# Kernel optimization log

Measured on AMD Instinct MI355X. Metric: run time of the kernel, lower is better.

## Reference

```python
import jax, jax.numpy as jnp
import numpy as np

MIN_RANGE = -128.0
MAX_RANGE = 127.0


def quantize(t, min_range=MIN_RANGE, max_range=MAX_RANGE):
    """Per-tensor affine (asymmetric) quantization, as in QuantizedMatrix.
    Returns (q, scale, zero_point) with q in [min_range, max_range]."""
    mn = jnp.min(t)
    mx = jnp.max(t)
    scale = (mx - mn) / (max_range - min_range)
    zero_point = jnp.round(min_range - mn / scale)
    q = jnp.clip(jnp.round(t / scale) + zero_point, min_range, max_range)
    return q, scale, zero_point


def setup_inputs() -> dict:
    key = jax.random.key(0)
    k1, k2, k3 = jax.random.split(key, 3)
    B, S, D_IN, D_OUT = 4, 2048, 4096, 4096
    x = jax.random.normal(k1, (B, S, D_IN), dtype=jnp.float32)
    # nn.Linear weight layout: [out_features, in_features]
    W = jax.random.normal(k2, (D_OUT, D_IN), dtype=jnp.float32) * (1.0 / np.sqrt(D_IN))
    bias = jax.random.normal(k3, (D_OUT,), dtype=jnp.float32) * 0.02
    return {"x": x, "W": W, "bias": bias}


def reference(x, W, bias):
    # Quantize activations (per-tensor over the whole [B,S,D] tensor) and weights.
    qx, sx, zx = quantize(x)
    qw, sw, zw = quantize(W)
    # QuantizedMatrix matmul: dequantized product
    #   s_x * s_w * (q_x - z_x) @ (q_w - z_w)^T  , W is [out,in] so contract on 'd'.
    acc = jnp.einsum("bsd,od->bso", qx - zx, qw - zw)
    res = (sx * sw) * acc + bias
    return res
```

## Files before the change

kernel.cpp:

```cpp
#include <hip/hip_runtime.h>

#define GM 8192
#define GN 4096
#define GK 4096
#define NT (GK / 64)

#define QX_OFF   0ull
#define QW_OFF   33554432ull
#define RSX_OFF  50331648ull
#define RSW_OFF  50364416ull
#define PRM_OFF  50380832ull

#define MMB_X 2048
#define MMB_W 1024

using v4i  = __attribute__((ext_vector_type(4)))  int;
using v16i = __attribute__((ext_vector_type(16))) int;

__device__ __forceinline__ void async16(const signed char* g, signed char* l) {
    __builtin_amdgcn_global_load_lds((const __attribute__((address_space(1))) void*)g,
                                     (__attribute__((address_space(3))) void*)l,
                                     16, 0, 0);
}

__global__ void k_minmax(const float4* __restrict__ x, const float4* __restrict__ Wt,
                         float* __restrict__ part) {
    const float4* p; int n4, b0, nb; float* dst;
    if (blockIdx.x < MMB_X) { p = x;  n4 = GM * GK / 4; b0 = blockIdx.x;         nb = MMB_X; dst = part;        }
    else                    { p = Wt; n4 = GN * GK / 4; b0 = blockIdx.x - MMB_X; nb = MMB_W; dst = part + 4096; }
    float mx = -3.4e38f, mn = 3.4e38f;
    for (int i = b0 * 256 + threadIdx.x; i < n4; i += nb * 256) {
        float4 v = p[i];
        mx = fmaxf(mx, fmaxf(fmaxf(v.x, v.y), fmaxf(v.z, v.w)));
        mn = fminf(mn, fminf(fminf(v.x, v.y), fminf(v.z, v.w)));
    }
    #pragma unroll
    for (int o = 32; o > 0; o >>= 1) {
        mx = fmaxf(mx, __shfl_down(mx, o));
        mn = fminf(mn, __shfl_down(mn, o));
    }
    __shared__ float smx[4], smn[4];
    int w = threadIdx.x >> 6;
    if ((threadIdx.x & 63) == 0) { smx[w] = mx; smn[w] = mn; }
    __syncthreads();
    if (threadIdx.x == 0) {
        #pragma unroll
        for (int i = 1; i < 4; i++) { mx = fmaxf(mx, smx[i]); mn = fminf(mn, smn[i]); }
        dst[b0]      = mx;
        dst[nb + b0] = mn;
    }
}

__global__ void k_params(const float* __restrict__ part, float* prm) {
    const int t = threadIdx.x;
    float v0 = -3.4e38f, v1 = 3.4e38f, v2 = -3.4e38f, v3 = 3.4e38f;
    for (int i = t; i < MMB_X; i += 256) {
        v0 = fmaxf(v0, part[i]);
        v1 = fminf(v1, part[MMB_X + i]);
    }
    for (int i = t; i < MMB_W; i += 256) {
        v2 = fmaxf(v2, part[4096 + i]);
        v3 = fminf(v3, part[5120 + i]);
    }
    #pragma unroll
    for (int o = 32; o > 0; o >>= 1) {
        v0 = fmaxf(v0, __shfl_down(v0, o));
        v1 = fminf(v1, __shfl_down(v1, o));
        v2 = fmaxf(v2, __shfl_down(v2, o));
        v3 = fminf(v3, __shfl_down(v3, o));
    }
    __shared__ float s[4][4];
    const int wv = t >> 6;
    if ((t & 63) == 0) { s[wv][0] = v0; s[wv][1] = v1; s[wv][2] = v2; s[wv][3] = v3; }
    __syncthreads();
    if (t == 0) {
        #pragma unroll
        for (int i = 1; i < 4; i++) {
            v0 = fmaxf(v0, s[i][0]); v1 = fminf(v1, s[i][1]);
            v2 = fmaxf(v2, s[i][2]); v3 = fminf(v3, s[i][3]);
        }
        float sx  = (v0 - v1) / 255.0f;
        float zxf = rintf(-128.0f - v1 / sx);
        float sw  = (v2 - v3) / 255.0f;
        float zwf = rintf(-128.0f - v3 / sw);
        prm[0] = sx; prm[1] = zxf; prm[2] = sw; prm[3] = zwf; prm[4] = sx * sw;
        int* ip = (int*)prm;
        ip[5] = (int)zxf; ip[6] = (int)zwf;
    }
}

__global__ void k_quant(const float* __restrict__ x, const float* __restrict__ Wt,
                        signed char* __restrict__ qx, signed char* __restrict__ qw,
                        int* __restrict__ rsx, int* __restrict__ rsw,
                        const float* __restrict__ prm) {
    const float* src; signed char* q; int* rs; int pidx, row;
    if (blockIdx.x < GM) { row = blockIdx.x;      src = x;  q = qx; rs = rsx; pidx = 0; }
    else                 { row = blockIdx.x - GM; src = Wt; q = qw; rs = rsw; pidx = 2; }
    const int t = threadIdx.x;
    const float s  = prm[pidx];
    const float zp = prm[pidx + 1];
    const float4* srow = (const float4*)(src + (size_t)row * GK);
    int* qrow = (int*)(q + (size_t)row * GK);
    int acc = 0;
    #pragma unroll
    for (int i = 0; i < 4; i++) {
        float4 v = srow[i * 256 + t];
        int q0 = (int)fminf(fmaxf(rintf(v.x / s) + zp, -128.0f), 127.0f);
        int q1 = (int)fminf(fmaxf(rintf(v.y / s) + zp, -128.0f), 127.0f);
        int q2 = (int)fminf(fmaxf(rintf(v.z / s) + zp, -128.0f), 127.0f);
        int q3 = (int)fminf(fmaxf(rintf(v.w / s) + zp, -128.0f), 127.0f);
        acc += q0 + q1 + q2 + q3;
        qrow[i * 256 + t] = (q0 & 255) | ((q1 & 255) << 8) | ((q2 & 255) << 16)
                          | ((q3 & 255) << 24);
    }
    #pragma unroll
    for (int o = 32; o > 0; o >>= 1) acc += __shfl_down(acc, o);
    __shared__ int sa[4];
    if ((t & 63) == 0) sa[t >> 6] = acc;
    __syncthreads();
    if (t == 0) rs[row] = sa[0] + sa[1] + sa[2] + sa[3];
}

__global__ __launch_bounds__(512, 2) void k_gemm(
    const signed char* __restrict__ qx, const signed char* __restrict__ qw,
    const int* __restrict__ rsx, const int* __restrict__ rsw,
    const float* __restrict__ bias, const float* __restrict__ prm,
    float* __restrict__ out) {
    __shared__ __align__(16) signed char lds[3][2][256 * 64];

    const int tid  = threadIdx.x;
    const int lane = tid & 63;
    const int w    = tid >> 6;
    const int bid  = ((blockIdx.x & 7) << 6) | (blockIdx.x >> 3);
    const int tm0  = (bid >> 4) * 256;
    const int tn0  = (bid & 15) * 256;

    const int slab = w & 3;
    const int sr   = lane >> 2;
    const int sc   = ((lane & 3) ^ ((lane >> 3) & 3)) * 16;
    const signed char* gsrc = (w < 4)
        ? qx + (size_t)(tm0 + slab * 64 + sr) * GK + sc
        : qw + (size_t)(tn0 + slab * 64 + sr) * GK + sc;
    const int ldsTensor = (w < 4) ? 0 : 1;
    const int ldsSlab   = slab * 64 * 64;

    const int wr = w >> 2;
    const int wc = w & 3;
    const int fr = lane & 31;
    const int fh = lane >> 5;

    v16i acc[4][2] = {};
    v4i  fa[4], fb[2];

    auto LDF = [&](int bi, int s) {
        const signed char* cA = lds[bi][0];
        const signed char* cB = lds[bi][1];
        const int cc = s * 2 + fh;
        const int ca = (cc ^ ((fr >> 1) & 3)) * 16;
        fa[0] = *(const v4i*)(cA + (wr * 128      + fr) * 64 + ca);
        fa[1] = *(const v4i*)(cA + (wr * 128 + 32 + fr) * 64 + ca);
        fa[2] = *(const v4i*)(cA + (wr * 128 + 64 + fr) * 64 + ca);
        fa[3] = *(const v4i*)(cA + (wr * 128 + 96 + fr) * 64 + ca);
        fb[0] = *(const v4i*)(cB + (wc * 64       + fr) * 64 + ca);
        fb[1] = *(const v4i*)(cB + (wc * 64  + 32 + fr) * 64 + ca);
    };
    auto MM = [&]() {
        __builtin_amdgcn_s_setprio(1);
        acc[0][0] = __builtin_amdgcn_mfma_i32_32x32x32_i8(fa[0], fb[0], acc[0][0], 0, 0, 0);
        acc[0][1] = __builtin_amdgcn_mfma_i32_32x32x32_i8(fa[0], fb[1], acc[0][1], 0, 0, 0);
        acc[1][0] = __builtin_amdgcn_mfma_i32_32x32x32_i8(fa[1], fb[0], acc[1][0], 0, 0, 0);
        acc[1][1] = __builtin_amdgcn_mfma_i32_32x32x32_i8(fa[1], fb[1], acc[1][1], 0, 0, 0);
        acc[2][0] = __builtin_amdgcn_mfma_i32_32x32x32_i8(fa[2], fb[0], acc[2][0], 0, 0, 0);
        acc[2][1] = __builtin_amdgcn_mfma_i32_32x32x32_i8(fa[2], fb[1], acc[2][1], 0, 0, 0);
        acc[3][0] = __builtin_amdgcn_mfma_i32_32x32x32_i8(fa[3], fb[0], acc[3][0], 0, 0, 0);
        acc[3][1] = __builtin_amdgcn_mfma_i32_32x32x32_i8(fa[3], fb[1], acc[3][1], 0, 0, 0);
        __builtin_amdgcn_s_setprio(0);
    };

    #pragma unroll
    for (int j = 0; j < 4; j++)
        async16(gsrc + (size_t)j * 16 * GK, &lds[0][ldsTensor][ldsSlab + j * 1024]);
    #pragma unroll
    for (int j = 0; j < 4; j++)
        async16(gsrc + (size_t)j * 16 * GK + 64, &lds[1][ldsTensor][ldsSlab + j * 1024]);
    asm volatile("s_waitcnt vmcnt(4)" ::: "memory");
    __builtin_amdgcn_s_barrier();
    LDF(0, 0);

    int rd = 0;
    for (int kt = 0; kt < NT; ++kt) {
        int st = rd + 2; if (st >= 3) st -= 3;
        const int nrd = (rd + 1 == 3) ? 0 : rd + 1;
        const size_t ko = (size_t)(kt + 2) * 64;
        const bool stg = (kt < NT - 2);
        __builtin_amdgcn_s_barrier();
        asm volatile("s_waitcnt lgkmcnt(0)" ::: "memory");
        __builtin_amdgcn_sched_barrier(0);
        MM();
        LDF(rd, 1);
        if (stg) {
            async16(gsrc + (size_t)0 * 16 * GK + ko, &lds[st][ldsTensor][ldsSlab + 0 * 1024]);
            async16(gsrc + (size_t)1 * 16 * GK + ko, &lds[st][ldsTensor][ldsSlab + 1 * 1024]);
            asm volatile("s_waitcnt vmcnt(2)" ::: "memory");
        } else if (kt == NT - 2) {
            asm volatile("s_waitcnt vmcnt(0)" ::: "memory");
        }
        __builtin_amdgcn_s_barrier();
        asm volatile("s_waitcnt lgkmcnt(0)" ::: "memory");
        __builtin_amdgcn_sched_barrier(0);
        MM();
        if (kt < NT - 1) LDF(nrd, 0);
        if (stg) {
            async16(gsrc + (size_t)2 * 16 * GK + ko, &lds[st][ldsTensor][ldsSlab + 2 * 1024]);
            async16(gsrc + (size_t)3 * 16 * GK + ko, &lds[st][ldsTensor][ldsSlab + 3 * 1024]);
        }
        rd = nrd;
    }

    const float sxsw = prm[4];
    const int* ip = (const int*)prm;
    const int zxi = ip[5], zwi = ip[6];
    const int kzz = GK * zxi * zwi;
    #pragma unroll
    for (int i = 0; i < 4; i++) {
        #pragma unroll
        for (int j = 0; j < 2; j++) {
            const int col = tn0 + wc * 64 + j * 32 + fr;
            const int ccol = kzz - zxi * rsw[col];
            const float bv = bias[col];
            #pragma unroll
            for (int reg = 0; reg < 16; reg++) {
                const int row = tm0 + wr * 128 + i * 32
                              + (reg & 3) + 8 * (reg >> 2) + 4 * fh;
                const int t = acc[i][j][reg] - zwi * rsx[row] + ccol;
                out[(size_t)row * GN + col] = fmaf(sxsw, (float)t, bv);
            }
        }
    }
}

extern "C" void kernel_launch(void* const* d_in, const int* in_sizes, int n_in,
                              void* d_out, int out_size, void* d_ws, size_t ws_size,
                              hipStream_t stream) {
    const float* x    = (const float*)d_in[0];
    const float* Wt   = (const float*)d_in[1];
    const float* bias = (const float*)d_in[2];
    float* out = (float*)d_out;

    char* ws = (char*)d_ws;
    signed char* qx = (signed char*)(ws + QX_OFF);
    signed char* qw = (signed char*)(ws + QW_OFF);
    int* rsx = (int*)(ws + RSX_OFF);
    int* rsw = (int*)(ws + RSW_OFF);
    float* part = (float*)(ws + QX_OFF);
    float* prm = (float*)(ws + PRM_OFF);

    k_minmax<<<MMB_X + MMB_W, 256, 0, stream>>>((const float4*)x, (const float4*)Wt, part);
    k_params<<<1, 256, 0, stream>>>(part, prm);
    k_quant<<<GM + GN, 256, 0, stream>>>(x, Wt, qx, qw, rsx, rsw, prm);
    k_gemm<<<(GM / 256) * (GN / 256), 512, 0, stream>>>(qx, qw, rsx, rsw, bias,
                                                        prm, out);
}
```

Baseline: 442.3 us.

## Shrink GEMM tile to 256x128 with 4 waves and simplify pipeline; wave-per-row quant

```diff
diff --git a/kernel.cpp b/kernel.cpp
--- a/kernel.cpp
+++ b/kernel.cpp
@@ -93,129 +93,112 @@
                         signed char* __restrict__ qx, signed char* __restrict__ qw,
                         int* __restrict__ rsx, int* __restrict__ rsw,
                         const float* __restrict__ prm) {
+    const int wid  = (blockIdx.x << 2) | (threadIdx.x >> 6);
+    const int lane = threadIdx.x & 63;
     const float* src; signed char* q; int* rs; int pidx, row;
-    if (blockIdx.x < GM) { row = blockIdx.x;      src = x;  q = qx; rs = rsx; pidx = 0; }
-    else                 { row = blockIdx.x - GM; src = Wt; q = qw; rs = rsw; pidx = 2; }
-    const int t = threadIdx.x;
+    if (wid < GM) { row = wid;      src = x;  q = qx; rs = rsx; pidx = 0; }
+    else          { row = wid - GM; src = Wt; q = qw; rs = rsw; pidx = 2; }
     const float s  = prm[pidx];
     const float zp = prm[pidx + 1];
     const float4* srow = (const float4*)(src + (size_t)row * GK);
     int* qrow = (int*)(q + (size_t)row * GK);
     int acc = 0;
     #pragma unroll
-    for (int i = 0; i < 4; i++) {
-        float4 v = srow[i * 256 + t];
+    for (int i = 0; i < 16; i++) {
+        float4 v = srow[i * 64 + lane];
         int q0 = (int)fminf(fmaxf(rintf(v.x / s) + zp, -128.0f), 127.0f);
         int q1 = (int)fminf(fmaxf(rintf(v.y / s) + zp, -128.0f), 127.0f);
         int q2 = (int)fminf(fmaxf(rintf(v.z / s) + zp, -128.0f), 127.0f);
         int q3 = (int)fminf(fmaxf(rintf(v.w / s) + zp, -128.0f), 127.0f);
         acc += q0 + q1 + q2 + q3;
-        qrow[i * 256 + t] = (q0 & 255) | ((q1 & 255) << 8) | ((q2 & 255) << 16)
-                          | ((q3 & 255) << 24);
+        qrow[i * 64 + lane] = (q0 & 255) | ((q1 & 255) << 8) | ((q2 & 255) << 16)
+                            | ((q3 & 255) << 24);
     }
     #pragma unroll
     for (int o = 32; o > 0; o >>= 1) acc += __shfl_down(acc, o);
-    __shared__ int sa[4];
-    if ((t & 63) == 0) sa[t >> 6] = acc;
-    __syncthreads();
-    if (t == 0) rs[row] = sa[0] + sa[1] + sa[2] + sa[3];
-}
-
-__global__ __launch_bounds__(512, 2) void k_gemm(
+    if (lane == 0) rs[row] = acc;
+}
+
+__global__ __launch_bounds__(256, 2) void k_gemm(
     const signed char* __restrict__ qx, const signed char* __restrict__ qw,
     const int* __restrict__ rsx, const int* __restrict__ rsw,
     const float* __restrict__ bias, const float* __restrict__ prm,
     float* __restrict__ out) {
-    __shared__ __align__(16) signed char lds[3][2][256 * 64];
+    __shared__ __align__(16) signed char lds[3][24576];
 
     const int tid  = threadIdx.x;
     const int lane = tid & 63;
     const int w    = tid >> 6;
-    const int bid  = ((blockIdx.x & 7) << 6) | (blockIdx.x >> 3);
-    const int tm0  = (bid >> 4) * 256;
-    const int tn0  = (bid & 15) * 256;
-
-    const int slab = w & 3;
-    const int sr   = lane >> 2;
-    const int sc   = ((lane & 3) ^ ((lane >> 3) & 3)) * 16;
-    const signed char* gsrc = (w < 4)
-        ? qx + (size_t)(tm0 + slab * 64 + sr) * GK + sc
-        : qw + (size_t)(tn0 + slab * 64 + sr) * GK + sc;
-    const int ldsTensor = (w < 4) ? 0 : 1;
-    const int ldsSlab   = slab * 64 * 64;
-
-    const int wr = w >> 2;
-    const int wc = w & 3;
+    const int bid  = ((blockIdx.x & 7) << 7) | (blockIdx.x >> 3);
+    const int tm0  = (bid >> 5) * 256;
+    const int tn0  = (bid & 31) * 128;
+
+    const int sr = lane >> 2;
+    const int sc = ((lane & 3) ^ ((lane >> 3) & 3)) * 16;
+    const signed char* gsg[6];
+    int lof[6];
+    #pragma unroll
+    for (int j6 = 0; j6 < 6; j6++) {
+        const int j = w * 6 + j6;
+        if (j < 16) { gsg[j6] = qx + (size_t)(tm0 + 16 * j        + sr) * GK + sc; lof[j6] = j * 1024; }
+        else        { gsg[j6] = qw + (size_t)(tn0 + 16 * (j - 16) + sr) * GK + sc; lof[j6] = 16384 + (j - 16) * 1024; }
+    }
+
+    const int wr = w >> 1;
+    const int wc = w & 1;
     const int fr = lane & 31;
     const int fh = lane >> 5;
 
     v16i acc[4][2] = {};
-    v4i  fa[4], fb[2];
-
-    auto LDF = [&](int bi, int s) {
-        const signed char* cA = lds[bi][0];
-        const signed char* cB = lds[bi][1];
-        const int cc = s * 2 + fh;
-        const int ca = (cc ^ ((fr >> 1) & 3)) * 16;
-        fa[0] = *(const v4i*)(cA + (wr * 128      + fr) * 64 + ca);
-        fa[1] = *(const v4i*)(cA + (wr * 128 + 32 + fr) * 64 + ca);
-        fa[2] = *(const v4i*)(cA + (wr * 128 + 64 + fr) * 64 + ca);
-        fa[3] = *(const v4i*)(cA + (wr * 128 + 96 + fr) * 64 + ca);
-        fb[0] = *(const v4i*)(cB + (wc * 64       + fr) * 64 + ca);
-        fb[1] = *(const v4i*)(cB + (wc * 64  + 32 + fr) * 64 + ca);
+
+    auto STAGE = [&](int buf, int kt) {
+        #pragma unroll
+        for (int j6 = 0; j6 < 6; j6++)
+            async16(gsg[j6] + (size_t)kt * 64, &lds[buf][lof[j6]]);
     };
-    auto MM = [&]() {
-        __builtin_amdgcn_s_setprio(1);
-        acc[0][0] = __builtin_amdgcn_mfma_i32_32x32x32_i8(fa[0], fb[0], acc[0][0], 0, 0, 0);
-        acc[0][1] = __builtin_amdgcn_mfma_i32_32x32x32_i8(fa[0], fb[1], acc[0][1], 0, 0, 0);
-        acc[1][0] = __builtin_amdgcn_mfma_i32_32x32x32_i8(fa[1], fb[0], acc[1][0], 0, 0, 0);
-        acc[1][1] = __builtin_amdgcn_mfma_i32_32x32x32_i8(fa[1], fb[1], acc[1][1], 0, 0, 0);
-        acc[2][0] = __builtin_amdgcn_mfma_i32_32x32x32_i8(fa[2], fb[0], acc[2][0], 0, 0, 0);
-        acc[2][1] = __builtin_amdgcn_mfma_i32_32x32x32_i8(fa[2], fb[1], acc[2][1], 0, 0, 0);
-        acc[3][0] = __builtin_amdgcn_mfma_i32_32x32x32_i8(fa[3], fb[0], acc[3][0], 0, 0, 0);
-        acc[3][1] = __builtin_amdgcn_mfma_i32_32x32x32_i8(fa[3], fb[1], acc[3][1], 0, 0, 0);
-        __builtin_amdgcn_s_setprio(0);
+    auto COMPUTE = [&](int rdi) {
+        const signed char* cA = lds[rdi];
+        const signed char* cB = lds[rdi] + 16384;
+        #pragma unroll
+        for (int s = 0; s < 2; s++) {
+            const int cc = s * 2 + fh;
+            const int ca = (cc ^ ((fr >> 1) & 3)) * 16;
+            v4i a0 = *(const v4i*)(cA + (wr * 128      + fr) * 64 + ca);
+            v4i a1 = *(const v4i*)(cA + (wr * 128 + 32 + fr) * 64 + ca);
+            v4i a2 = *(const v4i*)(cA + (wr * 128 + 64 + fr) * 64 + ca);
+            v4i a3 = *(const v4i*)(cA + (wr * 128 + 96 + fr) * 64 + ca);
+            v4i b0 = *(const v4i*)(cB + (wc * 64       + fr) * 64 + ca);
+            v4i b1 = *(const v4i*)(cB + (wc * 64  + 32 + fr) * 64 + ca);
+            acc[0][0] = __builtin_amdgcn_mfma_i32_32x32x32_i8(a0, b0, acc[0][0], 0, 0, 0);
+            acc[0][1] = __builtin_amdgcn_mfma_i32_32x32x32_i8(a0, b1, acc[0][1], 0, 0, 0);
+            acc[1][0] = __builtin_amdgcn_mfma_i32_32x32x32_i8(a1, b0, acc[1][0], 0, 0, 0);
+            acc[1][1] = __builtin_amdgcn_mfma_i32_32x32x32_i8(a1, b1, acc[1][1], 0, 0, 0);
+            acc[2][0] = __builtin_amdgcn_mfma_i32_32x32x32_i8(a2, b0, acc[2][0], 0, 0, 0);
+            acc[2][1] = __builtin_amdgcn_mfma_i32_32x32x32_i8(a2, b1, acc[2][1], 0, 0, 0);
+            acc[3][0] = __builtin_amdgcn_mfma_i32_32x32x32_i8(a3, b0, acc[3][0], 0, 0, 0);
+            acc[3][1] = __builtin_amdgcn_mfma_i32_32x32x32_i8(a3, b1, acc[3][1], 0, 0, 0);
+        }
     };
 
-    #pragma unroll
-    for (int j = 0; j < 4; j++)
-        async16(gsrc + (size_t)j * 16 * GK, &lds[0][ldsTensor][ldsSlab + j * 1024]);
-    #pragma unroll
-    for (int j = 0; j < 4; j++)
-        async16(gsrc + (size_t)j * 16 * GK + 64, &lds[1][ldsTensor][ldsSlab + j * 1024]);
-    asm volatile("s_waitcnt vmcnt(4)" ::: "memory");
+    STAGE(0, 0);
+    STAGE(1, 1);
+    asm volatile("s_waitcnt vmcnt(6)" ::: "memory");
     __builtin_amdgcn_s_barrier();
-    LDF(0, 0);
 
     int rd = 0;
-    for (int kt = 0; kt < NT; ++kt) {
+    for (int kt = 0; kt < NT - 2; ++kt) {
         int st = rd + 2; if (st >= 3) st -= 3;
-        const int nrd = (rd + 1 == 3) ? 0 : rd + 1;
-        const size_t ko = (size_t)(kt + 2) * 64;
-        const bool stg = (kt < NT - 2);
+        STAGE(st, kt + 2);
+        COMPUTE(rd);
+        asm volatile("s_waitcnt vmcnt(6)" ::: "memory");
         __builtin_amdgcn_s_barrier();
-        asm volatile("s_waitcnt lgkmcnt(0)" ::: "memory");
-        __builtin_amdgcn_sched_barrier(0);
-        MM();
-        LDF(rd, 1);
-        if (stg) {
-            async16(gsrc + (size_t)0 * 16 * GK + ko, &lds[st][ldsTensor][ldsSlab + 0 * 1024]);
-            async16(gsrc + (size_t)1 * 16 * GK + ko, &lds[st][ldsTensor][ldsSlab + 1 * 1024]);
-            asm volatile("s_waitcnt vmcnt(2)" ::: "memory");
-        } else if (kt == NT - 2) {
-            asm volatile("s_waitcnt vmcnt(0)" ::: "memory");
-        }
-        __builtin_amdgcn_s_barrier();
-        asm volatile("s_waitcnt lgkmcnt(0)" ::: "memory");
-        __builtin_amdgcn_sched_barrier(0);
-        MM();
-        if (kt < NT - 1) LDF(nrd, 0);
-        if (stg) {
-            async16(gsrc + (size_t)2 * 16 * GK + ko, &lds[st][ldsTensor][ldsSlab + 2 * 1024]);
-            async16(gsrc + (size_t)3 * 16 * GK + ko, &lds[st][ldsTensor][ldsSlab + 3 * 1024]);
-        }
-        rd = nrd;
-    }
+        rd = (rd + 1 == 3) ? 0 : rd + 1;
+    }
+    COMPUTE(rd);
+    asm volatile("s_waitcnt vmcnt(0)" ::: "memory");
+    __builtin_amdgcn_s_barrier();
+    rd = (rd + 1 == 3) ? 0 : rd + 1;
+    COMPUTE(rd);
 
     const float sxsw = prm[4];
     const int* ip = (const int*)prm;
@@ -257,7 +240,7 @@
 
     k_minmax<<<MMB_X + MMB_W, 256, 0, stream>>>((const float4*)x, (const float4*)Wt, part);
     k_params<<<1, 256, 0, stream>>>(part, prm);
-    k_quant<<<GM + GN, 256, 0, stream>>>(x, Wt, qx, qw, rsx, rsw, prm);
-    k_gemm<<<(GM / 256) * (GN / 256), 512, 0, stream>>>(qx, qw, rsx, rsw, bias,
+    k_quant<<<(GM + GN) / 4, 256, 0, stream>>>(x, Wt, qx, qw, rsx, rsw, prm);
+    k_gemm<<<(GM / 256) * (GN / 128), 256, 0, stream>>>(qx, qw, rsx, rsw, bias,
                                                         prm, out);
 }
```

Result: slower. 451.3 us (+2.0%).

## Restructure GEMM K-loop into four row-phases and use one wave per row in quantize

Applied to the files above, without the earlier changes.

```diff
diff --git a/kernel.cpp b/kernel.cpp
--- a/kernel.cpp
+++ b/kernel.cpp
@@ -93,32 +93,30 @@
                         signed char* __restrict__ qx, signed char* __restrict__ qw,
                         int* __restrict__ rsx, int* __restrict__ rsw,
                         const float* __restrict__ prm) {
+    const int wid  = (blockIdx.x << 2) | (threadIdx.x >> 6);
+    const int lane = threadIdx.x & 63;
     const float* src; signed char* q; int* rs; int pidx, row;
-    if (blockIdx.x < GM) { row = blockIdx.x;      src = x;  q = qx; rs = rsx; pidx = 0; }
-    else                 { row = blockIdx.x - GM; src = Wt; q = qw; rs = rsw; pidx = 2; }
-    const int t = threadIdx.x;
+    if (wid < GM) { row = wid;      src = x;  q = qx; rs = rsx; pidx = 0; }
+    else          { row = wid - GM; src = Wt; q = qw; rs = rsw; pidx = 2; }
     const float s  = prm[pidx];
     const float zp = prm[pidx + 1];
     const float4* srow = (const float4*)(src + (size_t)row * GK);
     int* qrow = (int*)(q + (size_t)row * GK);
     int acc = 0;
     #pragma unroll
-    for (int i = 0; i < 4; i++) {
-        float4 v = srow[i * 256 + t];
+    for (int i = 0; i < 16; i++) {
+        float4 v = srow[i * 64 + lane];
         int q0 = (int)fminf(fmaxf(rintf(v.x / s) + zp, -128.0f), 127.0f);
         int q1 = (int)fminf(fmaxf(rintf(v.y / s) + zp, -128.0f), 127.0f);
         int q2 = (int)fminf(fmaxf(rintf(v.z / s) + zp, -128.0f), 127.0f);
         int q3 = (int)fminf(fmaxf(rintf(v.w / s) + zp, -128.0f), 127.0f);
         acc += q0 + q1 + q2 + q3;
-        qrow[i * 256 + t] = (q0 & 255) | ((q1 & 255) << 8) | ((q2 & 255) << 16)
-                          | ((q3 & 255) << 24);
+        qrow[i * 64 + lane] = (q0 & 255) | ((q1 & 255) << 8) | ((q2 & 255) << 16)
+                            | ((q3 & 255) << 24);
     }
     #pragma unroll
     for (int o = 32; o > 0; o >>= 1) acc += __shfl_down(acc, o);
-    __shared__ int sa[4];
-    if ((t & 63) == 0) sa[t >> 6] = acc;
-    __syncthreads();
-    if (t == 0) rs[row] = sa[0] + sa[1] + sa[2] + sa[3];
+    if (lane == 0) rs[row] = acc;
 }
 
 __global__ __launch_bounds__(512, 2) void k_gemm(
@@ -150,32 +148,9 @@
     const int fh = lane >> 5;
 
     v16i acc[4][2] = {};
-    v4i  fa[4], fb[2];
-
-    auto LDF = [&](int bi, int s) {
-        const signed char* cA = lds[bi][0];
-        const signed char* cB = lds[bi][1];
-        const int cc = s * 2 + fh;
-        const int ca = (cc ^ ((fr >> 1) & 3)) * 16;
-        fa[0] = *(const v4i*)(cA + (wr * 128      + fr) * 64 + ca);
-        fa[1] = *(const v4i*)(cA + (wr * 128 + 32 + fr) * 64 + ca);
-        fa[2] = *(const v4i*)(cA + (wr * 128 + 64 + fr) * 64 + ca);
-        fa[3] = *(const v4i*)(cA + (wr * 128 + 96 + fr) * 64 + ca);
-        fb[0] = *(const v4i*)(cB + (wc * 64       + fr) * 64 + ca);
-        fb[1] = *(const v4i*)(cB + (wc * 64  + 32 + fr) * 64 + ca);
-    };
-    auto MM = [&]() {
-        __builtin_amdgcn_s_setprio(1);
-        acc[0][0] = __builtin_amdgcn_mfma_i32_32x32x32_i8(fa[0], fb[0], acc[0][0], 0, 0, 0);
-        acc[0][1] = __builtin_amdgcn_mfma_i32_32x32x32_i8(fa[0], fb[1], acc[0][1], 0, 0, 0);
-        acc[1][0] = __builtin_amdgcn_mfma_i32_32x32x32_i8(fa[1], fb[0], acc[1][0], 0, 0, 0);
-        acc[1][1] = __builtin_amdgcn_mfma_i32_32x32x32_i8(fa[1], fb[1], acc[1][1], 0, 0, 0);
-        acc[2][0] = __builtin_amdgcn_mfma_i32_32x32x32_i8(fa[2], fb[0], acc[2][0], 0, 0, 0);
-        acc[2][1] = __builtin_amdgcn_mfma_i32_32x32x32_i8(fa[2], fb[1], acc[2][1], 0, 0, 0);
-        acc[3][0] = __builtin_amdgcn_mfma_i32_32x32x32_i8(fa[3], fb[0], acc[3][0], 0, 0, 0);
-        acc[3][1] = __builtin_amdgcn_mfma_i32_32x32x32_i8(fa[3], fb[1], acc[3][1], 0, 0, 0);
-        __builtin_amdgcn_s_setprio(0);
-    };
+
+    const int ca0 = ((fh    ) ^ ((fr >> 1) & 3)) * 16;
+    const int ca1 = ((2 + fh) ^ ((fr >> 1) & 3)) * 16;
 
     #pragma unroll
     for (int j = 0; j < 4; j++)
@@ -185,36 +160,46 @@
         async16(gsrc + (size_t)j * 16 * GK + 64, &lds[1][ldsTensor][ldsSlab + j * 1024]);
     asm volatile("s_waitcnt vmcnt(4)" ::: "memory");
     __builtin_amdgcn_s_barrier();
-    LDF(0, 0);
 
     int rd = 0;
     for (int kt = 0; kt < NT; ++kt) {
         int st = rd + 2; if (st >= 3) st -= 3;
-        const int nrd = (rd + 1 == 3) ? 0 : rd + 1;
         const size_t ko = (size_t)(kt + 2) * 64;
         const bool stg = (kt < NT - 2);
-        __builtin_amdgcn_s_barrier();
-        asm volatile("s_waitcnt lgkmcnt(0)" ::: "memory");
-        __builtin_amdgcn_sched_barrier(0);
-        MM();
-        LDF(rd, 1);
-        if (stg) {
-            async16(gsrc + (size_t)0 * 16 * GK + ko, &lds[st][ldsTensor][ldsSlab + 0 * 1024]);
-            async16(gsrc + (size_t)1 * 16 * GK + ko, &lds[st][ldsTensor][ldsSlab + 1 * 1024]);
-            asm volatile("s_waitcnt vmcnt(2)" ::: "memory");
-        } else if (kt == NT - 2) {
-            asm volatile("s_waitcnt vmcnt(0)" ::: "memory");
+        const signed char* cA = lds[rd][0];
+        const signed char* cB = lds[rd][1];
+        v4i fb[2][2];
+        #pragma unroll
+        for (int p = 0; p < 4; ++p) {
+            const int ar = (wr * 128 + p * 32 + fr) * 64;
+            v4i fa0 = *(const v4i*)(cA + ar + ca0);
+            v4i fa1 = *(const v4i*)(cA + ar + ca1);
+            if (p == 0) {
+                const int br0 = (wc * 64      + fr) * 64;
+                const int br1 = (wc * 64 + 32 + fr) * 64;
+                fb[0][0] = *(const v4i*)(cB + br0 + ca0);
+                fb[0][1] = *(const v4i*)(cB + br0 + ca1);
+                fb[1][0] = *(const v4i*)(cB + br1 + ca0);
+                fb[1][1] = *(const v4i*)(cB + br1 + ca1);
+            }
+            if (stg)
+                async16(gsrc + (size_t)p * 16 * GK + ko,
+                        &lds[st][ldsTensor][ldsSlab + p * 1024]);
+            __builtin_amdgcn_s_barrier();
+            asm volatile("s_waitcnt lgkmcnt(0)" ::: "memory");
+            __builtin_amdgcn_s_setprio(1);
+            acc[p][0] = __builtin_amdgcn_mfma_i32_32x32x32_i8(fa0, fb[0][0], acc[p][0], 0, 0, 0);
+            acc[p][1] = __builtin_amdgcn_mfma_i32_32x32x32_i8(fa0, fb[1][0], acc[p][1], 0, 0, 0);
+            acc[p][0] = __builtin_amdgcn_mfma_i32_32x32x32_i8(fa1, fb[0][1], acc[p][0], 0, 0, 0);
+            acc[p][1] = __builtin_amdgcn_mfma_i32_32x32x32_i8(fa1, fb[1][1], acc[p][1], 0, 0, 0);
+            __builtin_amdgcn_s_setprio(0);
+            if (p == 3) {
+                if (stg)               asm volatile("s_waitcnt vmcnt(4)" ::: "memory");
+                else if (kt == NT - 2) asm volatile("s_waitcnt vmcnt(0)" ::: "memory");
+            }
+            __builtin_amdgcn_s_barrier();
         }
-        __builtin_amdgcn_s_barrier();
-        asm volatile("s_waitcnt lgkmcnt(0)" ::: "memory");
-        __builtin_amdgcn_sched_barrier(0);
-        MM();
-        if (kt < NT - 1) LDF(nrd, 0);
-        if (stg) {
-            async16(gsrc + (size_t)2 * 16 * GK + ko, &lds[st][ldsTensor][ldsSlab + 2 * 1024]);
-            async16(gsrc + (size_t)3 * 16 * GK + ko, &lds[st][ldsTensor][ldsSlab + 3 * 1024]);
-        }
-        rd = nrd;
+        rd = (rd + 1 == 3) ? 0 : rd + 1;
     }
 
     const float sxsw = prm[4];
@@ -257,7 +242,7 @@
 
     k_minmax<<<MMB_X + MMB_W, 256, 0, stream>>>((const float4*)x, (const float4*)Wt, part);
     k_params<<<1, 256, 0, stream>>>(part, prm);
-    k_quant<<<GM + GN, 256, 0, stream>>>(x, Wt, qx, qw, rsx, rsw, prm);
+    k_quant<<<(GM + GN) / 4, 256, 0, stream>>>(x, Wt, qx, qw, rsx, rsw, prm);
     k_gemm<<<(GM / 256) * (GN / 256), 512, 0, stream>>>(qx, qw, rsx, rsw, bias,
                                                         prm, out);
 }
```

New measurement: 441.8 us. About the same (-0.1%).
